# Kernel tuning notes

Measured on AMD Instinct MI355X. Metric: run time of the kernel, lower is better.

The kernel has to match this reference:

```python
import jax, jax.numpy as jnp
import numpy as np

HEADS = 16
DIM_HEAD = 64
SCALE = DIM_HEAD ** -0.5


def setup_inputs() -> dict:
    key = jax.random.key(0)
    ks = jax.random.split(key, 5)
    B, N, D = 2, 2048, 1024  # query_dim = inner_dim = 1024
    s = 0.02
    return {
        "x": jax.random.normal(ks[0], (B, N, D), dtype=jnp.float32),
        "Wq": jax.random.normal(ks[1], (D, D), dtype=jnp.float32) * s,
        "Wk": jax.random.normal(ks[2], (D, D), dtype=jnp.float32) * s,
        "Wv": jax.random.normal(ks[3], (D, D), dtype=jnp.float32) * s,
        "Wout": jax.random.normal(ks[4], (D, D), dtype=jnp.float32) * s,
        "bout": jnp.zeros((D,), dtype=jnp.float32),
    }


def reference(x, Wq, Wk, Wv, Wout, bout):
    B, N, D = x.shape
    h, dh = HEADS, DIM_HEAD
    # projections (torch Linear: y = x @ W.T); context = x (self-attention)
    q = (x @ Wq.T).reshape(B, N, h, dh).transpose(0, 2, 1, 3)  # b h n d
    k = (x @ Wk.T).reshape(B, N, h, dh).transpose(0, 2, 1, 3)
    v = (x @ Wv.T).reshape(B, N, h, dh).transpose(0, 2, 1, 3)
    # scaled dot-product attention; chunk loop in original is math-equivalent
    s = jnp.einsum('bhid,bhjd->bhij', q, k) * SCALE
    p = jax.nn.softmax(s, axis=-1)
    o = jnp.einsum('bhij,bhjd->bhid', p, v)  # b h n d
    o = o.transpose(0, 2, 1, 3).reshape(B, N, h * dh)
    return o @ Wout.T + bout
```

## Files before the change

kernel.cpp:

```cpp
#include <hip/hip_runtime.h>
#include <stdint.h>

using bf16x8 = __attribute__((ext_vector_type(8))) short;
using f32x4  = __attribute__((ext_vector_type(4))) float;
using s16x4  = __attribute__((ext_vector_type(4))) short;

__device__ __forceinline__ short f2bf(float f) {
    union { float f; uint32_t u; } v; v.f = f;
    uint32_t u = v.u;
    uint32_t r = (u + 0x7fffu + ((u >> 16) & 1u)) >> 16;
    return (short)r;
}

__device__ __forceinline__ uint32_t cvtpk_bf16(float a, float b) {
    uint32_t r;
    asm("v_cvt_pk_bf16_f32 %0, %1, %2" : "=v"(r) : "v"(a), "v"(b));
    return r;
}

__device__ __forceinline__ void gload_lds16(const void* g, void* l) {
    __builtin_amdgcn_global_load_lds(
        reinterpret_cast<const uint32_t __attribute__((address_space(1)))*>(
            reinterpret_cast<uintptr_t>(g)),
        reinterpret_cast<uint32_t __attribute__((address_space(3)))*>(
            reinterpret_cast<uintptr_t>(l)),
        16, 0, 0);
}

__global__ __launch_bounds__(256) void cvt_all(
    const float* __restrict__ x, const float* __restrict__ wq,
    const float* __restrict__ wk, const float* __restrict__ wv,
    const float* __restrict__ wo,
    short* __restrict__ xb, short* __restrict__ wqb, short* __restrict__ wkb,
    short* __restrict__ wvb, short* __restrict__ wob)
{
    int i = blockIdx.x * 256 + threadIdx.x;
    const float* src; short* dst; int off;
    if      (i < 1048576) { src = x;  dst = xb;  off = i; }
    else if (i < 1310720) { src = wq; dst = wqb; off = i - 1048576; }
    else if (i < 1572864) { src = wk; dst = wkb; off = i - 1310720; }
    else if (i < 1835008) { src = wv; dst = wvb; off = i - 1572864; }
    else                  { src = wo; dst = wob; off = i - 1835008; }
    float4 f = ((const float4*)src)[off];
    s16x4 r; r[0] = f2bf(f.x); r[1] = f2bf(f.y); r[2] = f2bf(f.z); r[3] = f2bf(f.w);
    ((s16x4*)dst)[off] = r;
}

template <bool IS_OUT>
__global__ __launch_bounds__(256) void gemm_bt(
    const short* __restrict__ A,
    const short* __restrict__ Bq, const short* __restrict__ Bk,
    const short* __restrict__ Bv,
    short* __restrict__ qb, short* __restrict__ kb, short* __restrict__ vtb,
    float* __restrict__ outp, const float* __restrict__ bias)
{
    constexpr int BN = IS_OUT ? 64 : 128;
    constexpr int BC = BN / 32;
    constexpr int NI = BN / 32;
    __shared__ short As[2][128 * 64];
    __shared__ short Bs[2][BN * 64];
    const int tid  = threadIdx.x;
    const int wave = tid >> 6, lane = tid & 63;
    const int lo = lane & 15, hi = lane >> 4;

    const int nwg = gridDim.x * gridDim.y * gridDim.z;
    int lin = blockIdx.x + blockIdx.y * gridDim.x +
              blockIdx.z * gridDim.x * gridDim.y;
    const int s = (lin & 7) * (nwg >> 3) + (lin >> 3);
    const int m_base = IS_OUT ? ((s >> 4) & 31) * 128 : ((s >> 3) & 31) * 128;
    const int n_base = IS_OUT ? (s & 15) * 64        : (s & 7) * 128;
    const int z = IS_OUT ? 0 : (s >> 8);

    const short* Bw = IS_OUT ? Bq : (z == 0 ? Bq : (z == 1 ? Bk : Bv));
    const int wr = wave >> 1, wc = wave & 1;

    f32x4 acc[4][NI];
#pragma unroll
    for (int i = 0; i < 4; ++i)
#pragma unroll
        for (int j = 0; j < NI; ++j) acc[i][j] = (f32x4){0.f, 0.f, 0.f, 0.f};

    const int se = (lane & 7) * 8;
    const short* Ag = A  + (size_t)(m_base + wave * 32 + (lane >> 3)) * 1024 + se;
    const short* Bg = Bw + (size_t)(n_base + wave * (BN / 4) + (lane >> 3)) * 1024 + se;

    auto GSTAGE = [&](int kt) {
        const int k0 = kt * 64, bf = kt & 1;
#pragma unroll
        for (int c = 0; c < 4; ++c)
            gload_lds16(Ag + (size_t)c * 8 * 1024 + k0, &As[bf][(wave * 32 + c * 8) * 64]);
#pragma unroll
        for (int c = 0; c < BC; ++c)
            gload_lds16(Bg + (size_t)c * 8 * 1024 + k0,
                        &Bs[bf][(wave * (BN / 4) + c * 8) * 64]);
    };

    GSTAGE(0);
    for (int kt = 0; kt < 16; ++kt) {
        if (kt < 15) {
            GSTAGE(kt + 1);
            if constexpr (IS_OUT)
                asm volatile("s_waitcnt vmcnt(6)" ::: "memory");
            else
                asm volatile("s_waitcnt vmcnt(8)" ::: "memory");
        } else {
            asm volatile("s_waitcnt vmcnt(0)" ::: "memory");
        }
        __builtin_amdgcn_s_barrier();
        const int bf = kt & 1;
#pragma unroll
        for (int ks = 0; ks < 2; ++ks) {
            bf16x8 av[4], bv[NI];
#pragma unroll
            for (int i = 0; i < 4; ++i)
                av[i] = *(const bf16x8*)&As[bf][(wr * 64 + i * 16 + lo) * 64 + ks * 32 + hi * 8];
#pragma unroll
            for (int i = 0; i < NI; ++i)
                bv[i] = *(const bf16x8*)&Bs[bf][(wc * (BN / 2) + i * 16 + lo) * 64 + ks * 32 + hi * 8];
#pragma unroll
            for (int mi = 0; mi < 4; ++mi)
#pragma unroll
                for (int ni = 0; ni < NI; ++ni)
                    acc[mi][ni] = __builtin_amdgcn_mfma_f32_16x16x32_bf16(
                        av[mi], bv[ni], acc[mi][ni], 0, 0, 0);
        }
        asm volatile("s_waitcnt lgkmcnt(0)" ::: "memory");
        __builtin_amdgcn_s_barrier();
    }

#pragma unroll
    for (int mi = 0; mi < 4; ++mi) {
#pragma unroll
        for (int ni = 0; ni < NI; ++ni) {
            const int n = n_base + wc * (BN / 2) + ni * 16 + lo;
            if (IS_OUT) {
                const float bsv = bias[n];
#pragma unroll
                for (int i = 0; i < 4; ++i) {
                    const int m = m_base + wr * 64 + mi * 16 + hi * 4 + i;
                    outp[(size_t)m * 1024 + n] = acc[mi][ni][i] + bsv;
                }
            } else {
                const int h = n >> 6, d = n & 63;
                if (z == 2) {
                    const int m0 = m_base + wr * 64 + mi * 16 + hi * 4;
                    const int b = m0 >> 11, ns = m0 & 2047;
                    s16x4 pk;
#pragma unroll
                    for (int i = 0; i < 4; ++i) pk[i] = f2bf(acc[mi][ni][i]);
                    *(s16x4*)&vtb[(((size_t)b * 16 + h) * 64 + d) * 2048 + ns] = pk;
                } else {
                    short* dstp = (z == 0) ? qb : kb;
                    const float scl = (z == 0) ? 0.18033688011112042f : 1.0f;
#pragma unroll
                    for (int i = 0; i < 4; ++i) {
                        const int m = m_base + wr * 64 + mi * 16 + hi * 4 + i;
                        const int b = m >> 11, ns = m & 2047;
                        dstp[(((size_t)b * 16 + h) * 2048 + ns) * 64 + d] =
                            f2bf(acc[mi][ni][i] * scl);
                    }
                }
            }
        }
    }
}


#define QKT16_(TT, S) do {                                                     \
    const char* kb_ = (const char*)K_lds[(TT) % 3];                            \
    bf16x8 kf_[4];                                                             \
    _Pragma("unroll")                                                          \
    for (int mi = 0; mi < 4; ++mi)                                             \
        kf_[mi] = *(const bf16x8*)(kb_ + (mi * 16 + lo) * 128 +                \
                                   ((hi ^ (lo & 7)) << 4));                    \
    _Pragma("unroll")                                                          \
    for (int mi = 0; mi < 4; ++mi)                                             \
        _Pragma("unroll")                                                      \
        for (int nf = 0; nf < 2; ++nf)                                         \
            S[mi][nf] = __builtin_amdgcn_mfma_f32_16x16x32_bf16(               \
                kf_[mi], qf[nf][0], Z4, 0, 0, 0);                              \
    _Pragma("unroll")                                                          \
    for (int mi = 0; mi < 4; ++mi)                                             \
        kf_[mi] = *(const bf16x8*)(kb_ + (mi * 16 + lo) * 128 +                \
                                   (((4 + hi) ^ (lo & 7)) << 4));              \
    _Pragma("unroll")                                                          \
    for (int mi = 0; mi < 4; ++mi)                                             \
        _Pragma("unroll")                                                      \
        for (int nf = 0; nf < 2; ++nf)                                         \
            S[mi][nf] = __builtin_amdgcn_mfma_f32_16x16x32_bf16(               \
                kf_[mi], qf[nf][1], S[mi][nf], 0, 0, 0);                       \
    } while (0)

#define HALF16_(T, SC, SN, DOQ) do {                                           \
    if ((T) < 30) {                                                            \
        STAGE((T) + 2);                                                        \
        asm volatile("s_waitcnt vmcnt(4)" ::: "memory");                       \
    } else {                                                                   \
        asm volatile("s_waitcnt vmcnt(0)" ::: "memory");                       \
    }                                                                          \
    __builtin_amdgcn_s_barrier();                                              \
    if (DOQ) {                                                                 \
        __builtin_amdgcn_s_setprio(1);                                         \
        QKT16_((T) + 1, SN);                                                   \
        __builtin_amdgcn_s_setprio(0);                                         \
    }                                                                          \
    __builtin_amdgcn_sched_barrier(0);      \
      \
    _Pragma("unroll")                                                          \
    for (int nf = 0; nf < 2; ++nf) {                                           \
        float s0 = 0.f, s1 = 0.f, s2 = 0.f, s3 = 0.f;                          \
        _Pragma("unroll")                                                      \
        for (int mi = 0; mi < 4; ++mi) {                                       \
            SC[mi][nf][0] = __builtin_amdgcn_exp2f(SC[mi][nf][0]);             \
            s0 += SC[mi][nf][0];                                               \
            SC[mi][nf][1] = __builtin_amdgcn_exp2f(SC[mi][nf][1]);             \
            s1 += SC[mi][nf][1];                                               \
            SC[mi][nf][2] = __builtin_amdgcn_exp2f(SC[mi][nf][2]);             \
            s2 += SC[mi][nf][2];                                               \
            SC[mi][nf][3] = __builtin_amdgcn_exp2f(SC[mi][nf][3]);             \
            s3 += SC[mi][nf][3];                                               \
        }                                                                      \
        lrow[nf] += (s0 + s1) + (s2 + s3);                                     \
    }                                                                          \
                 \
    _Pragma("unroll")                                                          \
    for (int nf = 0; nf < 2; ++nf)                                             \
        _Pragma("unroll")                                                      \
        for (int mi = 0; mi < 4; ++mi) {                                       \
            uint2 w;                                                           \
            w.x = cvtpk_bf16(SC[mi][nf][0], SC[mi][nf][1]);                    \
            w.y = cvtpk_bf16(SC[mi][nf][2], SC[mi][nf][3]);                    \
            const int row  = nf * 16 + lo;                                     \
            const int slot = (mi * 2 + (hi >> 1)) ^ (lo & 7);                  \
            *(uint2*)(pbase + row * 128 + (slot << 4) + (hi & 1) * 8) = w;     \
        }                                                                      \
    asm volatile("s_waitcnt lgkmcnt(0)" ::: "memory");                         \
    __builtin_amdgcn_sched_barrier(0);                                         \
           \
    __builtin_amdgcn_s_setprio(1);                                             \
    _Pragma("unroll")                                                          \
    for (int ks = 0; ks < 2; ++ks) {                                           \
        bf16x8 pa_[2], vf_[4];                                                 \
        _Pragma("unroll")                                                      \
        for (int mi = 0; mi < 2; ++mi)                                         \
            pa_[mi] = *(const bf16x8*)(pbase + (mi * 16 + lo) * 128 +          \
                                       (((ks * 4 + hi) ^ (lo & 7)) << 4));     \
        _Pragma("unroll")                                                      \
        for (int nf = 0; nf < 4; ++nf)                                         \
            vf_[nf] = *(const bf16x8*)((const char*)V_lds[(T) % 3] +           \
                                       (nf * 16 + lo) * 128 +                  \
                                       (((ks * 4 + hi) ^ (lo & 7)) << 4));     \
        _Pragma("unroll")                                                      \
        for (int mi = 0; mi < 2; ++mi)                                         \
            _Pragma("unroll")                                                  \
            for (int nf = 0; nf < 4; ++nf)                                     \
                oacc[mi][nf] = __builtin_amdgcn_mfma_f32_16x16x32_bf16(        \
                    pa_[mi], vf_[nf], oacc[mi][nf], 0, 0, 0);                  \
    }                                                                          \
    __builtin_amdgcn_s_setprio(0);                                             \
    asm volatile("s_waitcnt lgkmcnt(0)" ::: "memory");                         \
    __builtin_amdgcn_s_barrier();                                              \
    } while (0)

__global__ __launch_bounds__(256) void attn(
    const short* __restrict__ qg, const short* __restrict__ kg,
    const short* __restrict__ vtg, short* __restrict__ ob)
{
    __shared__ short K_lds[3][64 * 64];
    __shared__ short V_lds[3][64 * 64];
    __shared__ short P_lds[4 * 32 * 64];

    const int tid  = threadIdx.x;
    const int wave = tid >> 6, lane = tid & 63;
    const int lo = lane & 15, hi = lane >> 4;

    int bid = blockIdx.y * 16 + blockIdx.x;
    bid = (bid & 7) * 64 + (bid >> 3);
    const int bh = bid >> 4;
    const int qw = (bid & 15) * 128 + wave * 32;

    bf16x8 qf[2][2];
#pragma unroll
    for (int nf = 0; nf < 2; ++nf)
#pragma unroll
        for (int ks = 0; ks < 2; ++ks)
            qf[nf][ks] = *(const bf16x8*)&qg[((size_t)bh * 2048 + qw + nf * 16 + lo) * 64 +
                                             ks * 32 + hi * 8];
    asm volatile("s_waitcnt vmcnt(0)" ::: "memory");

    f32x4 oacc[2][4];
#pragma unroll
    for (int mi = 0; mi < 2; ++mi)
#pragma unroll
        for (int nf = 0; nf < 4; ++nf) oacc[mi][nf] = (f32x4){0.f, 0.f, 0.f, 0.f};
    float lrow[2] = {0.f, 0.f};
    const f32x4 Z4 = (f32x4){0.f, 0.f, 0.f, 0.f};

    char* pbase = (char*)P_lds + wave * 4096;
    const short* kgb = kg  + (size_t)bh * 2048 * 64;
    const short* vgb = vtg + (size_t)bh * 64 * 2048;

    const int stV = wave >> 1, rbase = (wave & 1) * 32;
    auto STAGE = [&](int t) {
        const int buf = t % 3, kv0 = t * 64;
#pragma unroll
        for (int c = 0; c < 4; ++c) {
            const int r  = rbase + c * 8 + (lane >> 3);
            const int sg = (lane & 7) ^ (r & 7);
            if (stV == 0)
                gload_lds16(kgb + (size_t)(kv0 + r) * 64 + sg * 8,
                            &K_lds[buf][(rbase + c * 8) * 64]);
            else
                gload_lds16(vgb + (size_t)r * 2048 + kv0 + sg * 8,
                            &V_lds[buf][(rbase + c * 8) * 64]);
        }
    };

    STAGE(0); STAGE(1);

    f32x4 sA[4][2], sB[4][2];

    asm volatile("s_waitcnt vmcnt(4)" ::: "memory");
    __builtin_amdgcn_s_barrier();
    QKT16_(0, sA);

    for (int u = 0; u < 15; ++u) {
        HALF16_(2 * u,     sA, sB, 1);
        HALF16_(2 * u + 1, sB, sA, 1);
    }
    HALF16_(30, sA, sB, 1);
    HALF16_(31, sB, sA, 0);

    float lfull[2];
#pragma unroll
    for (int nf = 0; nf < 2; ++nf) {
        float ts = lrow[nf];
        ts += __shfl_xor(ts, 16);
        ts += __shfl_xor(ts, 32);
        lfull[nf] = ts;
    }
    const int b = bh >> 4, h = bh & 15;
#pragma unroll
    for (int mi = 0; mi < 2; ++mi)
#pragma unroll
        for (int i = 0; i < 4; ++i) {
            const float lv = __shfl(lfull[mi], hi * 4 + i);
            const float r  = 1.0f / lv;
            const int qrow = qw + mi * 16 + hi * 4 + i;
#pragma unroll
            for (int nf = 0; nf < 4; ++nf)
                ob[((size_t)b * 2048 + qrow) * 1024 + h * 64 + nf * 16 + lo] =
                    f2bf(oacc[mi][nf][i] * r);
        }
}

extern "C" void kernel_launch(void* const* d_in, const int* in_sizes, int n_in,
                              void* d_out, int out_size, void* d_ws, size_t ws_size,
                              hipStream_t stream) {
    const float* x   = (const float*)d_in[0];
    const float* Wq  = (const float*)d_in[1];
    const float* Wk  = (const float*)d_in[2];
    const float* Wv  = (const float*)d_in[3];
    const float* Wo  = (const float*)d_in[4];
    const float* bo  = (const float*)d_in[5];
    float* outp = (float*)d_out;

    char* ws = (char*)d_ws;
    short* xb  = (short*)(ws);
    short* qb  = (short*)(ws + (8u  << 20));
    short* kb  = (short*)(ws + (16u << 20));
    short* vtb = (short*)(ws + (24u << 20));
    short* ob  = (short*)(ws + (32u << 20));
    short* wqb = (short*)(ws + (40u << 20));
    short* wkb = (short*)(ws + (42u << 20));
    short* wvb = (short*)(ws + (44u << 20));
    short* wob = (short*)(ws + (46u << 20));

    cvt_all<<<8192, 256, 0, stream>>>(x, Wq, Wk, Wv, Wo, xb, wqb, wkb, wvb, wob);
    gemm_bt<false><<<dim3(8, 32, 3), 256, 0, stream>>>(
        xb, wqb, wkb, wvb, qb, kb, vtb, nullptr, nullptr);
    attn<<<dim3(16, 32), 256, 0, stream>>>(qb, kb, vtb, ob);
    gemm_bt<true><<<dim3(16, 32, 1), 256, 0, stream>>>(
        ob, wob, nullptr, nullptr, nullptr, nullptr, nullptr, outp, bo);
}
```

Baseline: 143.9 us.

## Keep P in registers, halve per-wave query rows, add lazy online-softmax max

The attention kernel now gives each wave 16 query rows instead of 32 and launches twice as many blocks. The P tile stays in registers and is fed straight into the PV MFMA as the A operand, so the P_lds round trip and its waitcnt go away. V fragments are gathered as two 8-byte LDS reads to match the register layout. It also adds an online-softmax running max that rescales only when a new max exceeds the old one by more than 8 (in exp2 units), which guards against overflow at the cost of a max reduction and a vote per tile. With half the rows per wave, each K/V tile loaded into LDS is reused by fewer query rows, so more K/V traffic per unit of work is the tradeoff for higher occupancy and no P LDS traffic.

```diff
diff --git a/kernel.cpp b/kernel.cpp
--- a/kernel.cpp
+++ b/kernel.cpp
@@ -175,20 +175,16 @@
                                    ((hi ^ (lo & 7)) << 4));                    \
     _Pragma("unroll")                                                          \
     for (int mi = 0; mi < 4; ++mi)                                             \
-        _Pragma("unroll")                                                      \
-        for (int nf = 0; nf < 2; ++nf)                                         \
-            S[mi][nf] = __builtin_amdgcn_mfma_f32_16x16x32_bf16(               \
-                kf_[mi], qf[nf][0], Z4, 0, 0, 0);                              \
+        S[mi] = __builtin_amdgcn_mfma_f32_16x16x32_bf16(                       \
+            kf_[mi], qf0, Z4, 0, 0, 0);                                        \
     _Pragma("unroll")                                                          \
     for (int mi = 0; mi < 4; ++mi)                                             \
         kf_[mi] = *(const bf16x8*)(kb_ + (mi * 16 + lo) * 128 +                \
                                    (((4 + hi) ^ (lo & 7)) << 4));              \
     _Pragma("unroll")                                                          \
     for (int mi = 0; mi < 4; ++mi)                                             \
-        _Pragma("unroll")                                                      \
-        for (int nf = 0; nf < 2; ++nf)                                         \
-            S[mi][nf] = __builtin_amdgcn_mfma_f32_16x16x32_bf16(               \
-                kf_[mi], qf[nf][1], S[mi][nf], 0, 0, 0);                       \
+        S[mi] = __builtin_amdgcn_mfma_f32_16x16x32_bf16(                       \
+            kf_[mi], qf1, S[mi], 0, 0, 0);                                     \
     } while (0)
 
 #define HALF16_(T, SC, SN, DOQ) do {                                           \
@@ -204,58 +200,66 @@
         QKT16_((T) + 1, SN);                                                   \
         __builtin_amdgcn_s_setprio(0);                                         \
     }                                                                          \
-    __builtin_amdgcn_sched_barrier(0);      \
-      \
-    _Pragma("unroll")                                                          \
-    for (int nf = 0; nf < 2; ++nf) {                                           \
+        \
+    float pm_;                                                                 \
+    {                                                                          \
+        float a0 = fmaxf(fmaxf(SC[0][0], SC[0][1]), fmaxf(SC[0][2], SC[0][3]));\
+        float a1 = fmaxf(fmaxf(SC[1][0], SC[1][1]), fmaxf(SC[1][2], SC[1][3]));\
+        float a2 = fmaxf(fmaxf(SC[2][0], SC[2][1]), fmaxf(SC[2][2], SC[2][3]));\
+        float a3 = fmaxf(fmaxf(SC[3][0], SC[3][1]), fmaxf(SC[3][2], SC[3][3]));\
+        pm_ = fmaxf(fmaxf(a0, a1), fmaxf(a2, a3));                             \
+    }                                                                          \
+    if (!__all(pm_ <= mrow + 8.f)) {      \
+        float m4 = fmaxf(pm_, __shfl_xor(pm_, 16));                            \
+        m4 = fmaxf(m4, __shfl_xor(m4, 32));                                    \
+        const float mn = fmaxf(mrow, m4);                                      \
+        const float al_ = __builtin_amdgcn_exp2f(mrow - mn);                   \
+        mrow = mn; lrow *= al_;                                                \
+        _Pragma("unroll")                                                      \
+        for (int i = 0; i < 4; ++i) {                                          \
+            const float av = __shfl(al_, hi * 4 + i);                          \
+            _Pragma("unroll")                                                  \
+            for (int nf = 0; nf < 4; ++nf) oacc[nf][i] *= av;                  \
+        }                                                                      \
+    }                                                                          \
+    {                                       \
         float s0 = 0.f, s1 = 0.f, s2 = 0.f, s3 = 0.f;                          \
         _Pragma("unroll")                                                      \
         for (int mi = 0; mi < 4; ++mi) {                                       \
-            SC[mi][nf][0] = __builtin_amdgcn_exp2f(SC[mi][nf][0]);             \
-            s0 += SC[mi][nf][0];                                               \
-            SC[mi][nf][1] = __builtin_amdgcn_exp2f(SC[mi][nf][1]);             \
-            s1 += SC[mi][nf][1];                                               \
-            SC[mi][nf][2] = __builtin_amdgcn_exp2f(SC[mi][nf][2]);             \
-            s2 += SC[mi][nf][2];                                               \
-            SC[mi][nf][3] = __builtin_amdgcn_exp2f(SC[mi][nf][3]);             \
-            s3 += SC[mi][nf][3];                                               \
+            SC[mi][0] = __builtin_amdgcn_exp2f(SC[mi][0] - mrow); s0 += SC[mi][0]; \
+            SC[mi][1] = __builtin_amdgcn_exp2f(SC[mi][1] - mrow); s1 += SC[mi][1]; \
+            SC[mi][2] = __builtin_amdgcn_exp2f(SC[mi][2] - mrow); s2 += SC[mi][2]; \
+            SC[mi][3] = __builtin_amdgcn_exp2f(SC[mi][3] - mrow); s3 += SC[mi][3]; \
         }                                                                      \
-        lrow[nf] += (s0 + s1) + (s2 + s3);                                     \
+        lrow += (s0 + s1) + (s2 + s3);                                         \
     }                                                                          \
                  \
-    _Pragma("unroll")                                                          \
-    for (int nf = 0; nf < 2; ++nf)                                             \
+    uint32_t W_[4][2];                                                         \
+    _Pragma("unroll")                                                          \
+    for (int mi = 0; mi < 4; ++mi) {                                           \
+        W_[mi][0] = cvtpk_bf16(SC[mi][0], SC[mi][1]);                          \
+        W_[mi][1] = cvtpk_bf16(SC[mi][2], SC[mi][3]);                          \
+    }                                                                          \
+    \
+    __builtin_amdgcn_s_setprio(1);                                             \
+    _Pragma("unroll")                                                          \
+    for (int ks = 0; ks < 2; ++ks) {                                           \
+        union { uint32_t u[4]; bf16x8 v; } pk_;                                \
+        pk_.u[0] = W_[ks * 2][0];     pk_.u[1] = W_[ks * 2][1];                \
+        pk_.u[2] = W_[ks * 2 + 1][0]; pk_.u[3] = W_[ks * 2 + 1][1];            \
+        const char* vb_ = (const char*)V_lds[(T) % 3];                         \
+        const int g0_ = ((4 * ks +     (hi >> 1)) ^ (lo & 7)) << 4;            \
+        const int g1_ = ((4 * ks + 2 + (hi >> 1)) ^ (lo & 7)) << 4;            \
+        const int ib_ = (hi & 1) * 8;                                          \
         _Pragma("unroll")                                                      \
-        for (int mi = 0; mi < 4; ++mi) {                                       \
-            uint2 w;                                                           \
-            w.x = cvtpk_bf16(SC[mi][nf][0], SC[mi][nf][1]);                    \
-            w.y = cvtpk_bf16(SC[mi][nf][2], SC[mi][nf][3]);                    \
-            const int row  = nf * 16 + lo;                                     \
-            const int slot = (mi * 2 + (hi >> 1)) ^ (lo & 7);                  \
-            *(uint2*)(pbase + row * 128 + (slot << 4) + (hi & 1) * 8) = w;     \
+        for (int nf = 0; nf < 4; ++nf) {                                       \
+            const int rb_ = (nf * 16 + lo) * 128;                              \
+            union { uint2 h[2]; bf16x8 v; } vv_;                               \
+            vv_.h[0] = *(const uint2*)(vb_ + rb_ + g0_ + ib_);                 \
+            vv_.h[1] = *(const uint2*)(vb_ + rb_ + g1_ + ib_);                 \
+            oacc[nf] = __builtin_amdgcn_mfma_f32_16x16x32_bf16(                \
+                pk_.v, vv_.v, oacc[nf], 0, 0, 0);                              \
         }                                                                      \
-    asm volatile("s_waitcnt lgkmcnt(0)" ::: "memory");                         \
-    __builtin_amdgcn_sched_barrier(0);                                         \
-           \
-    __builtin_amdgcn_s_setprio(1);                                             \
-    _Pragma("unroll")                                                          \
-    for (int ks = 0; ks < 2; ++ks) {                                           \
-        bf16x8 pa_[2], vf_[4];                                                 \
-        _Pragma("unroll")                                                      \
-        for (int mi = 0; mi < 2; ++mi)                                         \
-            pa_[mi] = *(const bf16x8*)(pbase + (mi * 16 + lo) * 128 +          \
-                                       (((ks * 4 + hi) ^ (lo & 7)) << 4));     \
-        _Pragma("unroll")                                                      \
-        for (int nf = 0; nf < 4; ++nf)                                         \
-            vf_[nf] = *(const bf16x8*)((const char*)V_lds[(T) % 3] +           \
-                                       (nf * 16 + lo) * 128 +                  \
-                                       (((ks * 4 + hi) ^ (lo & 7)) << 4));     \
-        _Pragma("unroll")                                                      \
-        for (int mi = 0; mi < 2; ++mi)                                         \
-            _Pragma("unroll")                                                  \
-            for (int nf = 0; nf < 4; ++nf)                                     \
-                oacc[mi][nf] = __builtin_amdgcn_mfma_f32_16x16x32_bf16(        \
-                    pa_[mi], vf_[nf], oacc[mi][nf], 0, 0, 0);                  \
     }                                                                          \
     __builtin_amdgcn_s_setprio(0);                                             \
     asm volatile("s_waitcnt lgkmcnt(0)" ::: "memory");                         \
@@ -268,35 +272,27 @@
 {
     __shared__ short K_lds[3][64 * 64];
     __shared__ short V_lds[3][64 * 64];
-    __shared__ short P_lds[4 * 32 * 64];
 
     const int tid  = threadIdx.x;
     const int wave = tid >> 6, lane = tid & 63;
     const int lo = lane & 15, hi = lane >> 4;
 
-    int bid = blockIdx.y * 16 + blockIdx.x;
-    bid = (bid & 7) * 64 + (bid >> 3);
-    const int bh = bid >> 4;
-    const int qw = (bid & 15) * 128 + wave * 32;
-
-    bf16x8 qf[2][2];
-#pragma unroll
-    for (int nf = 0; nf < 2; ++nf)
-#pragma unroll
-        for (int ks = 0; ks < 2; ++ks)
-            qf[nf][ks] = *(const bf16x8*)&qg[((size_t)bh * 2048 + qw + nf * 16 + lo) * 64 +
-                                             ks * 32 + hi * 8];
+    int bid = blockIdx.y * 32 + blockIdx.x;
+    bid = (bid & 7) * 128 + (bid >> 3);
+    const int bh = bid >> 5;
+    const int qw = (bid & 31) * 64 + wave * 16;
+
+    bf16x8 qf0 = *(const bf16x8*)&qg[((size_t)bh * 2048 + qw + lo) * 64 + hi * 8];
+    bf16x8 qf1 = *(const bf16x8*)&qg[((size_t)bh * 2048 + qw + lo) * 64 + 32 + hi * 8];
     asm volatile("s_waitcnt vmcnt(0)" ::: "memory");
 
-    f32x4 oacc[2][4];
-#pragma unroll
-    for (int mi = 0; mi < 2; ++mi)
-#pragma unroll
-        for (int nf = 0; nf < 4; ++nf) oacc[mi][nf] = (f32x4){0.f, 0.f, 0.f, 0.f};
-    float lrow[2] = {0.f, 0.f};
+    f32x4 oacc[4];
+#pragma unroll
+    for (int nf = 0; nf < 4; ++nf) oacc[nf] = (f32x4){0.f, 0.f, 0.f, 0.f};
+    float mrow = -1e30f;
+    float lrow = 0.f;
     const f32x4 Z4 = (f32x4){0.f, 0.f, 0.f, 0.f};
 
-    char* pbase = (char*)P_lds + wave * 4096;
     const short* kgb = kg  + (size_t)bh * 2048 * 64;
     const short* vgb = vtg + (size_t)bh * 64 * 2048;
 
@@ -318,7 +314,7 @@
 
     STAGE(0); STAGE(1);
 
-    f32x4 sA[4][2], sB[4][2];
+    f32x4 sA[4], sB[4];
 
     asm volatile("s_waitcnt vmcnt(4)" ::: "memory");
     __builtin_amdgcn_s_barrier();
@@ -331,27 +327,20 @@
     HALF16_(30, sA, sB, 1);
     HALF16_(31, sB, sA, 0);
 
-    float lfull[2];
-#pragma unroll
-    for (int nf = 0; nf < 2; ++nf) {
-        float ts = lrow[nf];
-        ts += __shfl_xor(ts, 16);
-        ts += __shfl_xor(ts, 32);
-        lfull[nf] = ts;
+    float lfull = lrow;
+    lfull += __shfl_xor(lfull, 16);
+    lfull += __shfl_xor(lfull, 32);
+    const int b = bh >> 4, h = bh & 15;
+#pragma unroll
+    for (int i = 0; i < 4; ++i) {
+        const float lv = __shfl(lfull, hi * 4 + i);
+        const float r  = 1.0f / lv;
+        const int qrow = qw + hi * 4 + i;
+#pragma unroll
+        for (int nf = 0; nf < 4; ++nf)
+            ob[((size_t)b * 2048 + qrow) * 1024 + h * 64 + nf * 16 + lo] =
+                f2bf(oacc[nf][i] * r);
     }
-    const int b = bh >> 4, h = bh & 15;
-#pragma unroll
-    for (int mi = 0; mi < 2; ++mi)
-#pragma unroll
-        for (int i = 0; i < 4; ++i) {
-            const float lv = __shfl(lfull[mi], hi * 4 + i);
-            const float r  = 1.0f / lv;
-            const int qrow = qw + mi * 16 + hi * 4 + i;
-#pragma unroll
-            for (int nf = 0; nf < 4; ++nf)
-                ob[((size_t)b * 2048 + qrow) * 1024 + h * 64 + nf * 16 + lo] =
-                    f2bf(oacc[mi][nf][i] * r);
-        }
 }
 
 extern "C" void kernel_launch(void* const* d_in, const int* in_sizes, int n_in,
@@ -379,7 +368,7 @@
     cvt_all<<<8192, 256, 0, stream>>>(x, Wq, Wk, Wv, Wo, xb, wqb, wkb, wvb, wob);
     gemm_bt<false><<<dim3(8, 32, 3), 256, 0, stream>>>(
         xb, wqb, wkb, wvb, qb, kb, vtb, nullptr, nullptr);
-    attn<<<dim3(16, 32), 256, 0, stream>>>(qb, kb, vtb, ob);
+    attn<<<dim3(32, 32), 256, 0, stream>>>(qb, kb, vtb, ob);
     gemm_bt<true><<<dim3(16, 32, 1), 256, 0, stream>>>(
         ob, wob, nullptr, nullptr, nullptr, nullptr, nullptr, outp, bo);
 }
```

New measurement: 144.3 us. Within noise of the previous version (+0.3%).
